# Kernel optimization log

Hardware: AMD Instinct MI355X
Metric: run time of the kernel (lower is better)

The kernel has to match this reference:

```python
import jax, jax.numpy as jnp
import numpy as np

# dims: batch, seq_len(N)=hidden(H) (required: layer>0 feeds H back into Linears sized N),
# features C, AATE dim A, layers L, decoder widths
B, N, C, A, H, L, FC, FFC = 256, 512, 64, 64, 512, 3, 256, 32


def setup_inputs() -> dict:
    key = jax.random.key(0)
    ks = jax.random.split(key, 24)
    def p(k, shape):
        return jax.random.normal(k, shape, jnp.float32) * 0.02
    return dict(
        x=jax.random.normal(ks[0], (B, N, C), jnp.float32),
        occ=jax.random.normal(ks[1], (B, N, 1), jnp.float32),
        proj_w=p(ks[2], (A, N)), proj_b=p(ks[3], (A,)),
        ll1_w=p(ks[4], (L, A, N)), ll1_b=p(ks[5], (L, A)),
        ll2_w=p(ks[6], (L, A, N)), ll2_b=p(ks[7], (L, A)),
        g1_w=p(ks[8], (L, 1, N + A)), g1_b=p(ks[9], (L, 1)),
        g2_w=p(ks[10], (L, 1, N + A)), g2_b=p(ks[11], (L, 1)),
        gc_w=p(ks[12], (L, H, 3 * N)), gc_b=p(ks[13], (L, H)),
        ta_w=p(ks[14], (H, H)), ta_b=p(ks[15], (H,)),
        d1_w=p(ks[16], (FC, H)), d1_b=p(ks[17], (FC,)),
        d2_w=p(ks[18], (1, FC)), d2_b=p(ks[19], (1,)),
        c1_w=p(ks[20], (FFC, C)), c1_b=p(ks[21], (FFC,)),
        c2_w=p(ks[22], (1, FFC)), c2_b=p(ks[23], (1,)),
    )


def _nconv(x, a):
    # x: [B,F,n,m], a: [B,m,n,v] -> [B,F,v,m]   (torch.einsum('bfnm,bmnv->bfvm'))
    return jnp.einsum('bfnm,bmnv->bfvm', x, a)


def reference(x, occ, proj_w, proj_b, ll1_w, ll1_b, ll2_w, ll2_b,
              g1_w, g1_b, g2_w, g2_b, gc_w, gc_b, ta_w, ta_b,
              d1_w, d1_b, d2_w, d2_b, c1_w, c1_b, c2_w, c2_b):
    Bn, Nn, Cn = x.shape
    An = proj_w.shape[0]
    xm = jnp.transpose(x, (0, 2, 1))[:, :, None, :]               # [B,C,1,N]  (M=1)
    proj = jnp.transpose(occ, (0, 2, 1)) @ proj_w.T + proj_b      # [B,1,A]
    # torch: repeat(M,1,C,1).view(B,M,C,A) -> tile along C; view(B,M,A,C) reinterleaves
    AATE = jnp.tile(proj[:, :, None, :], (1, 1, Cn, 1))           # [B,1,C,A]
    AATE_T = AATE.reshape(Bn, 1, An, Cn)                          # [B,1,A,C] (raw reshape, as in torch .view)
    for l in range(L):
        a_pc = jnp.transpose(AATE, (0, 2, 1, 3))                  # [B,C,1,A]
        at_pc = jnp.transpose(AATE_T, (0, 3, 1, 2))               # [B,C,1,A]
        m1 = jax.nn.relu(jnp.tanh(jnp.concatenate([xm, a_pc], -1) @ g1_w[l].T + g1_b[l]))   # [B,C,1,1]
        m2 = jax.nn.relu(jnp.tanh(jnp.concatenate([xm, at_pc], -1) @ g2_w[l].T + g2_b[l]))  # [B,C,1,1]
        e1 = jax.nn.softmax(jax.nn.relu(m1 * (xm @ ll1_w[l].T + ll1_b[l])), axis=-1)        # [B,C,1,A]
        e2 = jax.nn.softmax(jax.nn.relu(m2 * (xm @ ll2_w[l].T + ll2_b[l])), axis=-1)        # [B,C,1,A]
        e1 = AATE + jnp.transpose(e1, (0, 2, 1, 3))               # [B,1,C,A]
        e2 = AATE_T + jnp.transpose(e2, (0, 2, 3, 1))             # [B,1,A,C]
        adp = jax.nn.softmax(jax.nn.relu(e1 @ e2), axis=-1)       # [B,1,C,C] adaptive adjacency
        xg = jnp.transpose(xm, (0, 3, 1, 2))                      # [B,N,C,1]
        x1 = _nconv(xg, adp)
        x2 = _nconv(x1, adp)
        h = jnp.concatenate([xg, x1, x2], axis=1)                 # [B,3N,C,1]
        hh = jnp.einsum('bfcm,of->bocm', h, gc_w[l]) + gc_b[l][None, :, None, None]  # [B,H,C,1]
        xnew = jnp.transpose(jax.nn.relu(hh), (0, 2, 3, 1))       # [B,C,1,H]
        xm = (xm + xnew) if l > 0 else xnew                       # residual for layer>0
    z = xm.mean(axis=2)                                           # [B,C,H]  (mean over M=1)
    z = z @ ta_w.T + ta_b                                         # temporal_agg (Linear)
    d = jax.nn.relu(z @ d1_w.T + d1_b) @ d2_w.T + d2_b            # decoder -> [B,C,1]
    dp = jnp.transpose(d, (0, 2, 1))                              # [B,1,C]
    cd = jax.nn.relu(dp @ c1_w.T + c1_b) @ c2_w.T + c2_b          # channel_decoder -> [B,1,1]
    return jnp.abs(jnp.transpose(cd, (0, 2, 1)).squeeze(-1))      # [B,1] rul_prediction
```

## Files before the change

### kernel.cpp

```cpp
#include <hip/hip_runtime.h>

typedef unsigned short u16;
typedef __attribute__((ext_vector_type(8))) short short8;
typedef __attribute__((ext_vector_type(4))) float f32x4;


__device__ __forceinline__ u16 f2b(float f) {
    union { float f; unsigned int i; } v; v.f = f;
    unsigned int x = v.i;
    x += 0x7fffu + ((x >> 16) & 1u);
    return (u16)(x >> 16);
}
__device__ __forceinline__ float b2f(u16 u) {
    union { unsigned int i; float f; } v;
    v.i = ((unsigned int)u) << 16;
    return v.f;
}
__device__ __forceinline__ void gl_lds16(const u16* g, u16* l) {
    __builtin_amdgcn_global_load_lds((__attribute__((address_space(1))) void*)(u16*)g,
                                     (__attribute__((address_space(3))) void*)l, 16, 0, 0);
}

__global__ __launch_bounds__(256) void k_cvt_all(const float* __restrict__ ll1w, const float* __restrict__ ll2w,
                                                 const float* __restrict__ gcw, const float* __restrict__ taw,
                                                 const float* __restrict__ d1w, u16* __restrict__ dst) {
    int i = blockIdx.x * 256 + threadIdx.x;
    if (i >= 737280) return;
    const float* src;
    int off;
    if (i < 24576)       { src = ll1w; off = i; }
    else if (i < 49152)  { src = ll2w; off = i - 24576; }
    else if (i < 638976) { src = gcw;  off = i - 49152; }
    else if (i < 704512) { src = taw;  off = i - 638976; }
    else                 { src = d1w;  off = i - 704512; }
    float4 v = ((const float4*)src)[off];
    ushort4 o; o.x = f2b(v.x); o.y = f2b(v.y); o.z = f2b(v.z); o.w = f2b(v.w);
    ((ushort4*)dst)[i] = o;
}

__global__ __launch_bounds__(256) void k_transpose(const float* __restrict__ x, u16* __restrict__ xmb) {
    __shared__ float tile[64][65];
    const int b  = blockIdx.y;
    const int n0 = blockIdx.x * 64;
    const int t  = threadIdx.x;
    const int c  = t & 63;
    const int dn = t >> 6;
#pragma unroll
    for (int i = 0; i < 16; ++i) {
        int nl = dn + i * 4;
        tile[c][nl] = x[((size_t)b * 512 + n0 + nl) * 64 + c];
    }
    __syncthreads();
    const int nl = t & 63;
    const int cb = (t >> 6) * 16;
#pragma unroll
    for (int i = 0; i < 16; ++i) {
        int c2 = cb + i;
        xmb[((size_t)b * 64 + c2) * 512 + n0 + nl] = f2b(tile[c2][nl]);
    }
}

__global__ __launch_bounds__(64) void k_proj(const float* __restrict__ occ, const float* __restrict__ pw,
                                             const float* __restrict__ pb, float* __restrict__ proj) {
    const int b = blockIdx.x;
    const int a = threadIdx.x;
    const float* ob = occ + (size_t)b * 512;
    const float* wr = pw + (size_t)a * 512;
    float acc = 0.f;
    for (int n = 0; n < 512; ++n) acc += ob[n] * wr[n];
    proj[b * 64 + a] = acc + pb[a];
}

__global__ __launch_bounds__(256) void k_pmadp(const u16* __restrict__ xmb, const float* __restrict__ vbuf,
                                               const float* __restrict__ g1w, const float* __restrict__ g1b,
                                               const float* __restrict__ g2w, const float* __restrict__ g2b,
                                               const float* __restrict__ proj, u16* __restrict__ adpT) {
    __shared__ float g1s[576], g2s[576], prj[64];
    __shared__ float P1s[64][64];
    __shared__ float P2s[64][65];
    __shared__ __align__(16) u16 Tl[64 * 72];
    const int b = blockIdx.x;
    const int t = threadIdx.x;
    const int lane = t & 63, w = t >> 6;
    if (t < 144) {
        *(float4*)&g1s[t * 4] = *(const float4*)(g1w + t * 4);
        *(float4*)&g2s[t * 4] = *(const float4*)(g2w + t * 4);
    }
    if (t >= 240) *(float4*)&prj[(t - 240) * 4] = *(const float4*)(proj + b * 64 + (t - 240) * 4);
    __syncthreads();
    float S1 = 0.f, G2 = 0.f;
#pragma unroll
    for (int a = 0; a < 64; ++a) { S1 += prj[a] * g1s[512 + a]; G2 += g2s[512 + a]; }
    const float b1 = g1b[0], b2v = g2b[0];
#pragma unroll 4
    for (int ci = 0; ci < 16; ++ci) {
        int c = w + ci * 4;
        int r = b * 64 + c;
        uint4 xv = *(const uint4*)(xmb + (size_t)r * 512 + lane * 8);
        const u16* xp = (const u16*)&xv;
        float a1 = 0.f, a2 = 0.f;
#pragma unroll
        for (int e = 0; e < 8; ++e) {
            float xf = b2f(xp[e]);
            a1 += xf * g1s[lane * 8 + e];
            a2 += xf * g2s[lane * 8 + e];
        }
        for (int off = 32; off; off >>= 1) { a1 += __shfl_xor(a1, off); a2 += __shfl_xor(a2, off); }
        float m1 = tanhf(a1 + S1 + b1);          m1 = m1 > 0.f ? m1 : 0.f;
        float m2 = tanhf(a2 + prj[c] * G2 + b2v); m2 = m2 > 0.f ? m2 : 0.f;
        float s1 = fmaxf(m1 * vbuf[(size_t)r * 128 + lane], 0.f);
        float s2 = fmaxf(m2 * vbuf[(size_t)r * 128 + 64 + lane], 0.f);
        float mx1 = s1, mx2 = s2;
        for (int off = 32; off; off >>= 1) { mx1 = fmaxf(mx1, __shfl_xor(mx1, off)); mx2 = fmaxf(mx2, __shfl_xor(mx2, off)); }
        float e1 = expf(s1 - mx1), e2 = expf(s2 - mx2);
        float su1 = e1, su2 = e2;
        for (int off = 32; off; off >>= 1) { su1 += __shfl_xor(su1, off); su2 += __shfl_xor(su2, off); }
        P1s[c][lane] = prj[lane] + e1 / su1;
        P2s[c][lane] = prj[c]    + e2 / su2;
    }
    __syncthreads();
    for (int ci = 0; ci < 16; ++ci) {
        int c = w + ci * 4;
        float s = 0.f;
        for (int a = 0; a < 64; ++a) s += P1s[c][a] * P2s[lane][a];
        s = fmaxf(s, 0.f);
        float mx = s;
        for (int off = 32; off; off >>= 1) mx = fmaxf(mx, __shfl_xor(mx, off));
        float e = expf(s - mx);
        float su = e;
        for (int off = 32; off; off >>= 1) su += __shfl_xor(su, off);
        Tl[lane * 72 + c] = f2b(e / su);
    }
    __syncthreads();
    const int v = t >> 2, ck = (t & 3) * 16;
    u16* dst = adpT + ((size_t)b * 64 + v) * 64 + ck;
    *(uint4*)dst       = *(const uint4*)&Tl[v * 72 + ck];
    *(uint4*)(dst + 8) = *(const uint4*)&Tl[v * 72 + ck + 8];
}

__global__ __launch_bounds__(256) void k_nconv2(const u16* __restrict__ Xbf, const u16* __restrict__ adpT,
                                                u16* __restrict__ x1bf, u16* __restrict__ x2bf) {
    __shared__ __align__(16) u16 Ts[64 * 72];
    __shared__ __align__(16) u16 Xs[128 * 72];
    const int b  = blockIdx.y;
    const int n0 = blockIdx.x * 128;
    const int t  = threadIdx.x;
    const int lane = t & 63, w = t >> 6;
    const int lrow = lane & 15, q = lane >> 4;
    const int wn = w * 32;

    {
        int v = t >> 2, ck = (t & 3) * 8;
        const u16* src = adpT + ((size_t)b * 64 + v) * 64;
        *(uint4*)&Ts[v * 72 + ck]      = *(const uint4*)(src + ck);
        *(uint4*)&Ts[v * 72 + ck + 32] = *(const uint4*)(src + ck + 32);
    }
    {
        int c = t >> 2;
        const u16* xr = Xbf + ((size_t)b * 64 + c) * 512 + n0;
#pragma unroll
        for (int j = 0; j < 4; ++j) {
            int nn = j * 32 + (t & 3) * 8;
            uint4 vv = *(const uint4*)(xr + nn);
            const u16* pv = (const u16*)&vv;
#pragma unroll
            for (int e = 0; e < 8; ++e) Xs[(nn + e) * 72 + c] = pv[e];
        }
    }
    __syncthreads();

    const f32x4 zero = {0.f, 0.f, 0.f, 0.f};
    f32x4 acc[4][2];
#pragma unroll
    for (int mt = 0; mt < 4; ++mt)
#pragma unroll
        for (int nt = 0; nt < 2; ++nt) acc[mt][nt] = zero;

#pragma unroll
    for (int ks = 0; ks < 2; ++ks) {
        short8 af[4], bfr[2];
#pragma unroll
        for (int mt = 0; mt < 4; ++mt) af[mt]  = *(const short8*)&Ts[(mt * 16 + lrow) * 72 + ks * 32 + q * 8];
#pragma unroll
        for (int nt = 0; nt < 2; ++nt) bfr[nt] = *(const short8*)&Xs[(wn + nt * 16 + lrow) * 72 + ks * 32 + q * 8];
#pragma unroll
        for (int mt = 0; mt < 4; ++mt)
#pragma unroll
            for (int nt = 0; nt < 2; ++nt)
                acc[mt][nt] = __builtin_amdgcn_mfma_f32_16x16x32_bf16(af[mt], bfr[nt], acc[mt][nt], 0, 0, 0);
    }
    __syncthreads();

#pragma unroll
    for (int mt = 0; mt < 4; ++mt)
#pragma unroll
        for (int nt = 0; nt < 2; ++nt) {
            int nl = wn + nt * 16 + lrow;
            ushort4 u;
            u.x = f2b(acc[mt][nt][0]); u.y = f2b(acc[mt][nt][1]);
            u.z = f2b(acc[mt][nt][2]); u.w = f2b(acc[mt][nt][3]);
            *(ushort4*)&Xs[nl * 72 + mt * 16 + q * 4] = u;
#pragma unroll
            for (int i = 0; i < 4; ++i)
                x1bf[((size_t)(b * 64 + mt * 16 + q * 4 + i)) * 512 + n0 + nl] = ((const u16*)&u)[i];
        }
    __syncthreads();

    f32x4 acc2[4][2];
#pragma unroll
    for (int mt = 0; mt < 4; ++mt)
#pragma unroll
        for (int nt = 0; nt < 2; ++nt) acc2[mt][nt] = zero;
#pragma unroll
    for (int ks = 0; ks < 2; ++ks) {
        short8 af[4], bfr[2];
#pragma unroll
        for (int mt = 0; mt < 4; ++mt) af[mt]  = *(const short8*)&Ts[(mt * 16 + lrow) * 72 + ks * 32 + q * 8];
#pragma unroll
        for (int nt = 0; nt < 2; ++nt) bfr[nt] = *(const short8*)&Xs[(wn + nt * 16 + lrow) * 72 + ks * 32 + q * 8];
#pragma unroll
        for (int mt = 0; mt < 4; ++mt)
#pragma unroll
            for (int nt = 0; nt < 2; ++nt)
                acc2[mt][nt] = __builtin_amdgcn_mfma_f32_16x16x32_bf16(af[mt], bfr[nt], acc2[mt][nt], 0, 0, 0);
    }
#pragma unroll
    for (int mt = 0; mt < 4; ++mt)
#pragma unroll
        for (int nt = 0; nt < 2; ++nt) {
            int nl = wn + nt * 16 + lrow;
#pragma unroll
            for (int i = 0; i < 4; ++i)
                x2bf[((size_t)(b * 64 + mt * 16 + q * 4 + i)) * 512 + n0 + nl] = f2b(acc2[mt][nt][i]);
        }
}

template<int BM, int BN>
__global__ __launch_bounds__(256) void mfma_gemm(
    const u16* __restrict__ A0, const u16* __restrict__ A1, const u16* __restrict__ A2,
    const u16* __restrict__ W0, const u16* __restrict__ W1, int nsplit,
    const float* __restrict__ bias0, const float* __restrict__ bias1,
    const u16* __restrict__ resbf, float* __restrict__ out, u16* __restrict__ outbf,
    int N, int K, int relu)
{
    constexpr int MT = BM / 32;
    constexpr int NT = BN / 32;
    constexpr int AI = BM / 16;
    constexpr int BI = BN / 16;
    constexpr int TILE = (BM + BN) * 32;
    __shared__ __align__(16) u16 SM[2 * TILE];
    const int t    = threadIdx.x;
    const int m0   = blockIdx.x * BM;
    const int n0   = blockIdx.y * BN;
    const int lane = t & 63;
    const int w    = t >> 6;
    const int wm   = (w >> 1) * (BM / 2);
    const int wn   = (w & 1) * (BN / 2);
    const int lrow = lane & 15;
    const int q    = lane >> 4;
    const int sr16 = lane >> 2;
    const int sp   = lane & 3;

    auto stage = [&](int k0, int buf) {
        u16* As = SM + buf * TILE;
        u16* Bs = As + BM * 32;
        const u16* Abase = A0;
        int kloc = k0;
        if (K > 512) {
            int seg = k0 >> 9;
            Abase = (seg == 0) ? A0 : ((seg == 1) ? A1 : A2);
            kloc = k0 & 511;
        }
#pragma unroll
        for (int jj = 0; jj < AI / 4; ++jj) {
            int j = jj * 4 + w;
            int row = j * 16 + sr16;
            int c = (sp - (row >> 1)) & 3;
            gl_lds16(Abase + (size_t)(m0 + row) * 512 + kloc + c * 8, As + j * 512);
        }
#pragma unroll
        for (int jj = 0; jj < BI / 4; ++jj) {
            int j = jj * 4 + w;
            int row = j * 16 + sr16;
            int n = n0 + row;
            const u16* wr = (n < nsplit) ? (W0 + (size_t)n * K) : (W1 + (size_t)(n - nsplit) * K);
            int c = (sp - (row >> 1)) & 3;
            gl_lds16(wr + k0 + c * 8, Bs + j * 512);
        }
    };

    const f32x4 zero = {0.f, 0.f, 0.f, 0.f};
    f32x4 acc[MT][NT];
#pragma unroll
    for (int i = 0; i < MT; ++i)
#pragma unroll
        for (int j = 0; j < NT; ++j) acc[i][j] = zero;

    stage(0, 0);
    const int iters = K >> 5;
    int buf = 0;
    for (int it = 0; it < iters; ++it) {
        __syncthreads();
        if (it + 1 < iters) stage((it + 1) * 32, buf ^ 1);
        const u16* As = SM + buf * TILE;
        const u16* Bs = As + BM * 32;
        short8 af[MT], bfr[NT];
#pragma unroll
        for (int mt = 0; mt < MT; ++mt) {
            int row = wm + mt * 16 + lrow;
            int p = (q + (row >> 1)) & 3;
            af[mt] = *(const short8*)&As[row * 32 + p * 8];
        }
#pragma unroll
        for (int nt = 0; nt < NT; ++nt) {
            int row = wn + nt * 16 + lrow;
            int p = (q + (row >> 1)) & 3;
            bfr[nt] = *(const short8*)&Bs[row * 32 + p * 8];
        }
#pragma unroll
        for (int mt = 0; mt < MT; ++mt)
#pragma unroll
            for (int nt = 0; nt < NT; ++nt)
                acc[mt][nt] = __builtin_amdgcn_mfma_f32_16x16x32_bf16(af[mt], bfr[nt], acc[mt][nt], 0, 0, 0);
        buf ^= 1;
    }

#pragma unroll
    for (int mt = 0; mt < MT; ++mt) {
        int mb = m0 + wm + mt * 16 + q * 4;
#pragma unroll
        for (int nt = 0; nt < NT; ++nt) {
            int n = n0 + wn + nt * 16 + lrow;
            float bvv = (n < nsplit) ? bias0[n] : bias1[n - nsplit];
#pragma unroll
            for (int i = 0; i < 4; ++i) {
                float v = acc[mt][nt][i] + bvv;
                if (relu) v = fmaxf(v, 0.f);
                if (resbf) v += b2f(resbf[(size_t)(mb + i) * N + n]);
                if (out) out[(size_t)(mb + i) * N + n] = v;
                if (outbf) outbf[(size_t)(mb + i) * N + n] = f2b(v);
            }
        }
    }
}

__global__ __launch_bounds__(256) void k_dec(const float* __restrict__ x2T, const float* __restrict__ d2w,
                                             const float* __restrict__ d2b, const float* __restrict__ c1w,
                                             const float* __restrict__ c1b, const float* __restrict__ c2w,
                                             const float* __restrict__ c2b, float* __restrict__ out) {
    __shared__ float dv[64];
    __shared__ float d2s[256];
    const int b = blockIdx.x, t = threadIdx.x;
    const int lane = t & 63, w = t >> 6;
    if (t < 64) *(float4*)&d2s[t * 4] = *(const float4*)(d2w + t * 4);
    __syncthreads();
#pragma unroll 4
    for (int ci = 0; ci < 16; ++ci) {
        int c = w + ci * 4;
        const float* row = x2T + (size_t)(b * 64 + c) * 256;
        float acc = row[lane] * d2s[lane] + row[64 + lane] * d2s[64 + lane]
                  + row[128 + lane] * d2s[128 + lane] + row[192 + lane] * d2s[192 + lane];
        for (int off = 32; off; off >>= 1) acc += __shfl_xor(acc, off);
        if (lane == 0) dv[c] = acc + d2b[0];
    }
    __syncthreads();
    if (w == 0) {
        float part = 0.f;
        if (lane < 32) {
            float acc = c1b[lane];
            for (int c = 0; c < 64; ++c) acc += dv[c] * c1w[lane * 64 + c];
            part = fmaxf(acc, 0.f) * c2w[lane];
        }
        for (int off = 32; off; off >>= 1) part += __shfl_xor(part, off);
        if (lane == 0) out[b] = fabsf(part + c2b[0]);
    }
}

extern "C" void kernel_launch(void* const* d_in, const int* in_sizes, int n_in,
                              void* d_out, int out_size, void* d_ws, size_t ws_size,
                              hipStream_t stream) {
    const float* x     = (const float*)d_in[0];
    const float* occ   = (const float*)d_in[1];
    const float* projw = (const float*)d_in[2];
    const float* projb = (const float*)d_in[3];
    const float* ll1w  = (const float*)d_in[4];
    const float* ll1b  = (const float*)d_in[5];
    const float* ll2w  = (const float*)d_in[6];
    const float* ll2b  = (const float*)d_in[7];
    const float* g1w   = (const float*)d_in[8];
    const float* g1b   = (const float*)d_in[9];
    const float* g2w   = (const float*)d_in[10];
    const float* g2b   = (const float*)d_in[11];
    const float* gcw   = (const float*)d_in[12];
    const float* gcb   = (const float*)d_in[13];
    const float* taw   = (const float*)d_in[14];
    const float* tab   = (const float*)d_in[15];
    const float* d1w   = (const float*)d_in[16];
    const float* d1b   = (const float*)d_in[17];
    const float* d2w   = (const float*)d_in[18];
    const float* d2b   = (const float*)d_in[19];
    const float* c1w   = (const float*)d_in[20];
    const float* c1b   = (const float*)d_in[21];
    const float* c2w   = (const float*)d_in[22];
    const float* c2b   = (const float*)d_in[23];

    const size_t MR = (size_t)16384 * 512;
    float* ws   = (float*)d_ws;
    float* x2T  = ws;
    float* vbuf = x2T + (size_t)16384 * 256;
    float* proj = vbuf + (size_t)16384 * 128;
    u16* bfb     = (u16*)(proj + 16384);
    u16* xmA_bf  = bfb;
    u16* xmB_bf  = xmA_bf + MR;
    u16* x1_bf   = xmB_bf + MR;
    u16* x2_bf   = x1_bf + MR;
    u16* x1T_bf  = x2_bf + MR;
    u16* adpT_bf = x1T_bf + MR;
    u16* wb      = adpT_bf + (size_t)16384 * 64;
    u16* ll1w_bf = wb;
    u16* ll2w_bf = ll1w_bf + 98304;
    u16* gcw_bf  = ll2w_bf + 98304;
    u16* taw_bf  = gcw_bf + 2359296;
    u16* d1w_bf  = taw_bf + 262144;

    k_cvt_all<<<2880, 256, 0, stream>>>(ll1w, ll2w, gcw, taw, d1w, wb);
    k_transpose<<<dim3(8, 256), 256, 0, stream>>>(x, xmA_bf);
    k_proj<<<256, 64, 0, stream>>>(occ, projw, projb, proj);

    u16* cur_bf = xmA_bf;
    u16* nxt_bf = xmB_bf;
    for (int l = 0; l < 3; ++l) {
        mfma_gemm<64, 64><<<dim3(256, 2), 256, 0, stream>>>(
            cur_bf, nullptr, nullptr,
            ll1w_bf + (size_t)l * 32768, ll2w_bf + (size_t)l * 32768, 64,
            ll1b + l * 64, ll2b + l * 64, nullptr, vbuf, nullptr, 128, 512, 0);
        k_pmadp<<<256, 256, 0, stream>>>(cur_bf, vbuf, g1w + l * 576, g1b + l,
                                         g2w + l * 576, g2b + l, proj, adpT_bf);
        k_nconv2<<<dim3(4, 256), 256, 0, stream>>>(cur_bf, adpT_bf, x1_bf, x2_bf);
        mfma_gemm<128, 64><<<dim3(128, 8), 256, 0, stream>>>(
            cur_bf, x1_bf, x2_bf,
            gcw_bf + (size_t)l * 786432, gcw_bf + (size_t)l * 786432, 512,
            gcb + l * 512, gcb + l * 512, (l > 0 ? cur_bf : nullptr), nullptr, nxt_bf, 512, 1536, 1);
        { u16* tb = cur_bf; cur_bf = nxt_bf; nxt_bf = tb; }
    }
    mfma_gemm<128, 64><<<dim3(128, 8), 256, 0, stream>>>(
        cur_bf, nullptr, nullptr, taw_bf, taw_bf, 512, tab, tab, nullptr, nullptr, x1T_bf, 512, 512, 0);
    mfma_gemm<64, 64><<<dim3(256, 4), 256, 0, stream>>>(
        x1T_bf, nullptr, nullptr, d1w_bf, d1w_bf, 256, d1b, d1b, nullptr, x2T, nullptr, 256, 512, 1);
    k_dec<<<256, 256, 0, stream>>>(x2T, d2w, d2b, c1w, c1b, c2w, c2b, (float*)d_out);
}
```

Baseline: 468.9 us.

## Split adjacency kernel into per-row gating kernel and MFMA-based softmax adjacency kernel

The fused per-batch k_pmadp kernel is replaced by two kernels. k_pm runs one 64-thread block per (batch, channel) row to compute the gated softmax vectors, giving far more parallelism, and writes them to a new bf16 buffer. k_adp2 then computes the 64x64 P1·P2ᵀ product with bf16 MFMA instead of scalar FP32 loops, followed by a row softmax done with shuffles. Separately, k_nconv2's X transpose into LDS now uses 4-channel packed ushort4 stores instead of scalar u16 stores. Costs are an extra launch, a global round trip for P, and bf16 rounding of P before the product.

```diff
diff --git a/kernel.cpp b/kernel.cpp
--- a/kernel.cpp
+++ b/kernel.cpp
@@ -71,66 +71,91 @@
     proj[b * 64 + a] = acc + pb[a];
 }
 
-__global__ __launch_bounds__(256) void k_pmadp(const u16* __restrict__ xmb, const float* __restrict__ vbuf,
-                                               const float* __restrict__ g1w, const float* __restrict__ g1b,
-                                               const float* __restrict__ g2w, const float* __restrict__ g2b,
-                                               const float* __restrict__ proj, u16* __restrict__ adpT) {
-    __shared__ float g1s[576], g2s[576], prj[64];
-    __shared__ float P1s[64][64];
-    __shared__ float P2s[64][65];
+__global__ __launch_bounds__(64) void k_pm(const u16* __restrict__ xmb, const float* __restrict__ vb,
+                                           const float* __restrict__ g1w, const float* __restrict__ g1b,
+                                           const float* __restrict__ g2w, const float* __restrict__ g2b,
+                                           const float* __restrict__ proj, u16* __restrict__ Pb) {
+    const int r = blockIdx.x;
+    const int b = r >> 6, c = r & 63;
+    const int lane = threadIdx.x;
+    uint4 xv = *(const uint4*)(xmb + (size_t)r * 512 + lane * 8);
+    const u16* xp = (const u16*)&xv;
+    float4 w1a = *(const float4*)(g1w + lane * 8);
+    float4 w1b = *(const float4*)(g1w + lane * 8 + 4);
+    float4 w2a = *(const float4*)(g2w + lane * 8);
+    float4 w2b = *(const float4*)(g2w + lane * 8 + 4);
+    float g1v[8] = {w1a.x, w1a.y, w1a.z, w1a.w, w1b.x, w1b.y, w1b.z, w1b.w};
+    float g2v[8] = {w2a.x, w2a.y, w2a.z, w2a.w, w2b.x, w2b.y, w2b.z, w2b.w};
+    float a1 = 0.f, a2 = 0.f;
+#pragma unroll
+    for (int e = 0; e < 8; ++e) {
+        float xf = b2f(xp[e]);
+        a1 += xf * g1v[e];
+        a2 += xf * g2v[e];
+    }
+    a1 += proj[b * 64 + lane] * g1w[512 + lane];
+    a2 += proj[b * 64 + c]    * g2w[512 + lane];
+    for (int off = 32; off; off >>= 1) { a1 += __shfl_xor(a1, off); a2 += __shfl_xor(a2, off); }
+    float m1 = tanhf(a1 + g1b[0]); m1 = m1 > 0.f ? m1 : 0.f;
+    float m2 = tanhf(a2 + g2b[0]); m2 = m2 > 0.f ? m2 : 0.f;
+    const int a = lane;
+    float s1 = fmaxf(m1 * vb[(size_t)r * 128 + a], 0.f);
+    float s2 = fmaxf(m2 * vb[(size_t)r * 128 + 64 + a], 0.f);
+    float mx1 = s1, mx2 = s2;
+    for (int off = 32; off; off >>= 1) { mx1 = fmaxf(mx1, __shfl_xor(mx1, off)); mx2 = fmaxf(mx2, __shfl_xor(mx2, off)); }
+    float e1 = expf(s1 - mx1), e2 = expf(s2 - mx2);
+    float su1 = e1, su2 = e2;
+    for (int off = 32; off; off >>= 1) { su1 += __shfl_xor(su1, off); su2 += __shfl_xor(su2, off); }
+    Pb[(size_t)r * 128 + a]      = f2b(proj[b * 64 + a] + e1 / su1);
+    Pb[(size_t)r * 128 + 64 + a] = f2b(proj[b * 64 + c] + e2 / su2);
+}
+
+__global__ __launch_bounds__(256) void k_adp2(const u16* __restrict__ Pb, u16* __restrict__ adpT) {
+    __shared__ __align__(16) u16 P1s[64 * 72];
+    __shared__ __align__(16) u16 P2s[64 * 72];
     __shared__ __align__(16) u16 Tl[64 * 72];
-    const int b = blockIdx.x;
-    const int t = threadIdx.x;
+    const int b = blockIdx.x, t = threadIdx.x;
     const int lane = t & 63, w = t >> 6;
-    if (t < 144) {
-        *(float4*)&g1s[t * 4] = *(const float4*)(g1w + t * 4);
-        *(float4*)&g2s[t * 4] = *(const float4*)(g2w + t * 4);
-    }
-    if (t >= 240) *(float4*)&prj[(t - 240) * 4] = *(const float4*)(proj + b * 64 + (t - 240) * 4);
-    __syncthreads();
-    float S1 = 0.f, G2 = 0.f;
-#pragma unroll
-    for (int a = 0; a < 64; ++a) { S1 += prj[a] * g1s[512 + a]; G2 += g2s[512 + a]; }
-    const float b1 = g1b[0], b2v = g2b[0];
-#pragma unroll 4
-    for (int ci = 0; ci < 16; ++ci) {
-        int c = w + ci * 4;
-        int r = b * 64 + c;
-        uint4 xv = *(const uint4*)(xmb + (size_t)r * 512 + lane * 8);
-        const u16* xp = (const u16*)&xv;
-        float a1 = 0.f, a2 = 0.f;
-#pragma unroll
-        for (int e = 0; e < 8; ++e) {
-            float xf = b2f(xp[e]);
-            a1 += xf * g1s[lane * 8 + e];
-            a2 += xf * g2s[lane * 8 + e];
-        }
-        for (int off = 32; off; off >>= 1) { a1 += __shfl_xor(a1, off); a2 += __shfl_xor(a2, off); }
-        float m1 = tanhf(a1 + S1 + b1);          m1 = m1 > 0.f ? m1 : 0.f;
-        float m2 = tanhf(a2 + prj[c] * G2 + b2v); m2 = m2 > 0.f ? m2 : 0.f;
-        float s1 = fmaxf(m1 * vbuf[(size_t)r * 128 + lane], 0.f);
-        float s2 = fmaxf(m2 * vbuf[(size_t)r * 128 + 64 + lane], 0.f);
-        float mx1 = s1, mx2 = s2;
-        for (int off = 32; off; off >>= 1) { mx1 = fmaxf(mx1, __shfl_xor(mx1, off)); mx2 = fmaxf(mx2, __shfl_xor(mx2, off)); }
-        float e1 = expf(s1 - mx1), e2 = expf(s2 - mx2);
-        float su1 = e1, su2 = e2;
-        for (int off = 32; off; off >>= 1) { su1 += __shfl_xor(su1, off); su2 += __shfl_xor(su2, off); }
-        P1s[c][lane] = prj[lane] + e1 / su1;
-        P2s[c][lane] = prj[c]    + e2 / su2;
-    }
-    __syncthreads();
-    for (int ci = 0; ci < 16; ++ci) {
-        int c = w + ci * 4;
-        float s = 0.f;
-        for (int a = 0; a < 64; ++a) s += P1s[c][a] * P2s[lane][a];
-        s = fmaxf(s, 0.f);
-        float mx = s;
-        for (int off = 32; off; off >>= 1) mx = fmaxf(mx, __shfl_xor(mx, off));
-        float e = expf(s - mx);
-        float su = e;
-        for (int off = 32; off; off >>= 1) su += __shfl_xor(su, off);
-        Tl[lane * 72 + c] = f2b(e / su);
-    }
+    const int lrow = lane & 15, q = lane >> 4;
+    {
+        int rr = t >> 2, ck = (t & 3) * 16;
+        const u16* src = Pb + ((size_t)b * 64 + rr) * 128;
+        *(uint4*)&P1s[rr * 72 + ck]     = *(const uint4*)(src + ck);
+        *(uint4*)&P1s[rr * 72 + ck + 8] = *(const uint4*)(src + ck + 8);
+        *(uint4*)&P2s[rr * 72 + ck]     = *(const uint4*)(src + 64 + ck);
+        *(uint4*)&P2s[rr * 72 + ck + 8] = *(const uint4*)(src + 64 + ck + 8);
+    }
+    __syncthreads();
+    const f32x4 zero = {0.f, 0.f, 0.f, 0.f};
+    short8 a0 = *(const short8*)&P1s[(w * 16 + lrow) * 72 + q * 8];
+    short8 a1 = *(const short8*)&P1s[(w * 16 + lrow) * 72 + 32 + q * 8];
+    f32x4 s[4];
+#pragma unroll
+    for (int nt = 0; nt < 4; ++nt) {
+        short8 b0 = *(const short8*)&P2s[(nt * 16 + lrow) * 72 + q * 8];
+        short8 b1 = *(const short8*)&P2s[(nt * 16 + lrow) * 72 + 32 + q * 8];
+        s[nt] = __builtin_amdgcn_mfma_f32_16x16x32_bf16(a0, b0, zero, 0, 0, 0);
+        s[nt] = __builtin_amdgcn_mfma_f32_16x16x32_bf16(a1, b1, s[nt], 0, 0, 0);
+    }
+    float mx[4], su[4];
+#pragma unroll
+    for (int i = 0; i < 4; ++i) {
+        float m = 0.f;
+#pragma unroll
+        for (int nt = 0; nt < 4; ++nt) { s[nt][i] = fmaxf(s[nt][i], 0.f); m = fmaxf(m, s[nt][i]); }
+        for (int off = 1; off < 16; off <<= 1) m = fmaxf(m, __shfl_xor(m, off));
+        mx[i] = m;
+        float e = 0.f;
+#pragma unroll
+        for (int nt = 0; nt < 4; ++nt) { s[nt][i] = expf(s[nt][i] - m); e += s[nt][i]; }
+        for (int off = 1; off < 16; off <<= 1) e += __shfl_xor(e, off);
+        su[i] = e;
+    }
+#pragma unroll
+    for (int nt = 0; nt < 4; ++nt)
+#pragma unroll
+        for (int i = 0; i < 4; ++i)
+            Tl[(nt * 16 + lrow) * 72 + (w * 16 + q * 4 + i)] = f2b(s[nt][i] / su[i]);
     __syncthreads();
     const int v = t >> 2, ck = (t & 3) * 16;
     u16* dst = adpT + ((size_t)b * 64 + v) * 64 + ck;
@@ -156,15 +181,18 @@
         *(uint4*)&Ts[v * 72 + ck + 32] = *(const uint4*)(src + ck + 32);
     }
     {
-        int c = t >> 2;
-        const u16* xr = Xbf + ((size_t)b * 64 + c) * 512 + n0;
-#pragma unroll
-        for (int j = 0; j < 4; ++j) {
-            int nn = j * 32 + (t & 3) * 8;
-            uint4 vv = *(const uint4*)(xr + nn);
-            const u16* pv = (const u16*)&vv;
-#pragma unroll
-            for (int e = 0; e < 8; ++e) Xs[(nn + e) * 72 + c] = pv[e];
+        int nn8 = (t >> 4) * 8;
+        int cb  = (t & 15) * 4;
+        const u16* xr = Xbf + ((size_t)(b * 64 + cb)) * 512 + n0 + nn8;
+        uint4 v0 = *(const uint4*)(xr);
+        uint4 v1 = *(const uint4*)(xr + 512);
+        uint4 v2 = *(const uint4*)(xr + 1024);
+        uint4 v3 = *(const uint4*)(xr + 1536);
+        const u16 *p0 = (const u16*)&v0, *p1 = (const u16*)&v1, *p2 = (const u16*)&v2, *p3 = (const u16*)&v3;
+#pragma unroll
+        for (int e = 0; e < 8; ++e) {
+            ushort4 pk; pk.x = p0[e]; pk.y = p1[e]; pk.z = p2[e]; pk.w = p3[e];
+            *(ushort4*)&Xs[(nn8 + e) * 72 + cb] = pk;
         }
     }
     __syncthreads();
@@ -416,7 +444,8 @@
     u16* x2_bf   = x1_bf + MR;
     u16* x1T_bf  = x2_bf + MR;
     u16* adpT_bf = x1T_bf + MR;
-    u16* wb      = adpT_bf + (size_t)16384 * 64;
+    u16* Pb_bf   = adpT_bf + (size_t)16384 * 64;
+    u16* wb      = Pb_bf + (size_t)16384 * 128;
     u16* ll1w_bf = wb;
     u16* ll2w_bf = ll1w_bf + 98304;
     u16* gcw_bf  = ll2w_bf + 98304;
@@ -434,8 +463,9 @@
             cur_bf, nullptr, nullptr,
             ll1w_bf + (size_t)l * 32768, ll2w_bf + (size_t)l * 32768, 64,
             ll1b + l * 64, ll2b + l * 64, nullptr, vbuf, nullptr, 128, 512, 0);
-        k_pmadp<<<256, 256, 0, stream>>>(cur_bf, vbuf, g1w + l * 576, g1b + l,
-                                         g2w + l * 576, g2b + l, proj, adpT_bf);
+        k_pm<<<16384, 64, 0, stream>>>(cur_bf, vbuf, g1w + l * 576, g1b + l,
+                                       g2w + l * 576, g2b + l, proj, Pb_bf);
+        k_adp2<<<256, 256, 0, stream>>>(Pb_bf, adpT_bf);
         k_nconv2<<<dim3(4, 256), 256, 0, stream>>>(cur_bf, adpT_bf, x1_bf, x2_bf);
         mfma_gemm<128, 64><<<dim3(128, 8), 256, 0, stream>>>(
             cur_bf, x1_bf, x2_bf,
```

New measurement: 418.7 us. 1.12x faster.
